# Kernel tuning notes

Measured on AMD Instinct MI355X. Metric: run time of the kernel, lower is better.

Reference implementation:

```python
import jax, jax.numpy as jnp
import numpy as np

B, L, H, E, D = 2, 2048, 8, 64, 64

def setup_inputs() -> dict:
    key = jax.random.key(0)
    kq, kk, kv, ks = jax.random.split(key, 4)
    return {
        "queries": jax.random.normal(kq, (B, L, H, E), dtype=jnp.float32),
        "keys": jax.random.normal(kk, (B, L, H, E), dtype=jnp.float32),
        "values": jax.random.normal(kv, (B, L, H, D), dtype=jnp.float32),
        "sigma": jax.random.normal(ks, (B, L, H), dtype=jnp.float32),
    }

def reference(queries, keys, values, sigma):
    b, l, h, e = queries.shape
    scale = 1.0 / np.sqrt(e).astype(np.float32)
    # raw attention scores [B,H,L,S]
    scores = jnp.einsum('blhe,bshe->bhls', queries, keys)
    # strict causal mask (mask j > i)
    causal = jnp.triu(jnp.ones((l, l), dtype=bool), k=1)
    scores = jnp.where(causal[None, None], -jnp.inf, scores)
    attn = scale * scores
    # learned Gaussian prior per query-key distance
    sig = jnp.transpose(sigma, (0, 2, 1))            # [B,H,L]
    sig = jax.nn.sigmoid(sig * 5.0) + 1e-5
    sig = jnp.power(3.0, sig) - 1.0                  # in (0, 2)
    sig = sig[..., None]                             # [B,H,L,1] broadcast over window
    idx = jnp.arange(l, dtype=jnp.float32)
    dist = jnp.abs(idx[:, None] - idx[None, :])      # [L,L]
    inv_sqrt_2pi = 1.0 / np.sqrt(2.0 * np.pi).astype(np.float32)
    prior = (inv_sqrt_2pi / sig) * jnp.exp(-(dist[None, None] ** 2) / (2.0 * sig ** 2))  # [B,H,L,L]
    series = jax.nn.softmax(attn, axis=-1)           # [B,H,L,S]
    V = jnp.einsum('bhls,bshd->blhd', series, values)  # [B,L,H,D]
    sigma_out = jnp.broadcast_to(sig, prior.shape)
    return V, series, prior, sigma_out
```

## Files before the change

kernel.cpp:

```cpp
#include <hip/hip_runtime.h>

#define B_ 2
#define L_ 2048
#define H_ 8
#define E_ 64

typedef __attribute__((ext_vector_type(8))) short short8;
typedef __attribute__((ext_vector_type(4))) float f32x4;

static constexpr size_t OFF_S = 2097152;
static constexpr size_t OFF_P = OFF_S + 67108864;
static constexpr size_t OFF_G = OFF_P + 67108864;

__device__ __forceinline__ unsigned short f2bf(float x) {
    union { float f; unsigned int u; } c; c.f = x;
    unsigned int u = c.u;
    u += 0x7fffu + ((u >> 16) & 1u);
    return (unsigned short)(u >> 16);
}

__device__ __forceinline__ void st_bf4(unsigned short* dst, float4 x) {
    union { unsigned short u[4]; uint2 v; } t;
    t.u[0] = f2bf(x.x); t.u[1] = f2bf(x.y); t.u[2] = f2bf(x.z); t.u[3] = f2bf(x.w);
    *reinterpret_cast<uint2*>(dst) = t.v;
}

__global__ __launch_bounds__(256) void attn_all(
    const float* __restrict__ q, const float* __restrict__ k,
    const float* __restrict__ v, const float* __restrict__ sg,
    float* __restrict__ out)
{
    __shared__ __attribute__((aligned(16))) unsigned short Ks[64][72];
    __shared__ __attribute__((aligned(16))) unsigned short Vt[64][72];
    __shared__ __attribute__((aligned(16))) unsigned short Pt[16][72];
    __shared__ float l_sums[16];
    __shared__ float rowA[16], rowC[16], rowSig[16];

    const int tid  = threadIdx.x;
    const int wv   = tid >> 6;
    const int lane = tid & 63;
    const int quad = lane >> 4;
    const int l16  = lane & 15;

    const int blk = blockIdx.x;
    const int s   = 127 - (blk >> 4);
    const int bh  = blk & 15;
    const int b   = bh >> 3;
    const int h   = bh & 7;
    const int i0  = s << 4;

    if (tid < 16) l_sums[tid] = 0.0f;

    short8 a0, a1;
    {
        const float* qr = q + ((size_t)((b * L_ + (i0 + l16)) * H_ + h)) * E_;
        const float4* q4 = reinterpret_cast<const float4*>(qr) + quad * 2;
        float4 x0 = q4[0], x1 = q4[1];
        float4 y0 = q4[8], y1 = q4[9];
        union { short8 v8; unsigned short u[8]; } fa, fb;
        fa.u[0]=f2bf(x0.x); fa.u[1]=f2bf(x0.y); fa.u[2]=f2bf(x0.z); fa.u[3]=f2bf(x0.w);
        fa.u[4]=f2bf(x1.x); fa.u[5]=f2bf(x1.y); fa.u[6]=f2bf(x1.z); fa.u[7]=f2bf(x1.w);
        fb.u[0]=f2bf(y0.x); fb.u[1]=f2bf(y0.y); fb.u[2]=f2bf(y0.z); fb.u[3]=f2bf(y0.w);
        fb.u[4]=f2bf(y1.x); fb.u[5]=f2bf(y1.y); fb.u[6]=f2bf(y1.z); fb.u[7]=f2bf(y1.w);
        a0 = fa.v8; a1 = fb.v8;
    }

    const int ntiles = ((i0 + 15) >> 6) + 1;
    const int jend   = ntiles << 6;

    float lpart[4] = {0.f, 0.f, 0.f, 0.f};
    for (int t = 0; t < ntiles; ++t) {
        const int j0 = t << 6;
        __syncthreads();
        {
            int r = tid >> 4;
            const int c = (tid & 15) << 2;
            #pragma unroll
            for (int p = 0; p < 4; ++p, r += 16) {
                const size_t g = ((size_t)((b * L_ + (j0 + r)) * H_ + h)) * E_ + c;
                st_bf4(&Ks[r][c], *reinterpret_cast<const float4*>(k + g));
            }
        }
        __syncthreads();
        const unsigned short* krow = &Ks[(wv << 4) + l16][0];
        short8 b0 = *reinterpret_cast<const short8*>(krow + quad * 8);
        short8 b1 = *reinterpret_cast<const short8*>(krow + 32 + quad * 8);
        f32x4 c4 = {0.f, 0.f, 0.f, 0.f};
        c4 = __builtin_amdgcn_mfma_f32_16x16x32_bf16(a0, b0, c4, 0, 0, 0);
        c4 = __builtin_amdgcn_mfma_f32_16x16x32_bf16(a1, b1, c4, 0, 0, 0);
        const int j = j0 + (wv << 4) + l16;
        #pragma unroll
        for (int r = 0; r < 4; ++r) {
            const int i = i0 + (quad << 2) + r;
            lpart[r] += (j <= i) ? __expf(c4[r] * 0.125f - 8.0f) : 0.0f;
        }
    }
    #pragma unroll
    for (int r = 0; r < 4; ++r) {
        float x = lpart[r];
        x += __shfl_xor(x, 1); x += __shfl_xor(x, 2);
        x += __shfl_xor(x, 4); x += __shfl_xor(x, 8);
        if (l16 == 0) atomicAdd(&l_sums[(quad << 2) + r], x);
    }
    __syncthreads();
    float inv[4];
    #pragma unroll
    for (int r = 0; r < 4; ++r) inv[r] = 1.0f / l_sums[(quad << 2) + r];

    f32x4 oacc = {0.f, 0.f, 0.f, 0.f};
    float* outS = out + OFF_S;
    for (int t = 0; t < ntiles; ++t) {
        const int j0 = t << 6;
        __syncthreads();
        {
            int r = tid >> 4;
            const int c = (tid & 15) << 2;
            #pragma unroll
            for (int p = 0; p < 4; ++p, r += 16) {
                const size_t g = ((size_t)((b * L_ + (j0 + r)) * H_ + h)) * E_ + c;
                st_bf4(&Ks[r][c], *reinterpret_cast<const float4*>(k + g));
                const float4 vv = *reinterpret_cast<const float4*>(v + g);
                Vt[c + 0][r] = f2bf(vv.x);
                Vt[c + 1][r] = f2bf(vv.y);
                Vt[c + 2][r] = f2bf(vv.z);
                Vt[c + 3][r] = f2bf(vv.w);
            }
        }
        __syncthreads();
        const unsigned short* krow = &Ks[(wv << 4) + l16][0];
        short8 b0 = *reinterpret_cast<const short8*>(krow + quad * 8);
        short8 b1 = *reinterpret_cast<const short8*>(krow + 32 + quad * 8);
        f32x4 c4 = {0.f, 0.f, 0.f, 0.f};
        c4 = __builtin_amdgcn_mfma_f32_16x16x32_bf16(a0, b0, c4, 0, 0, 0);
        c4 = __builtin_amdgcn_mfma_f32_16x16x32_bf16(a1, b1, c4, 0, 0, 0);
        const int j = j0 + (wv << 4) + l16;
        #pragma unroll
        for (int r = 0; r < 4; ++r) {
            const int i = i0 + (quad << 2) + r;
            float p = (j <= i) ? __expf(c4[r] * 0.125f - 8.0f) : 0.0f;
            float pn = p * inv[r];
            outS[((size_t)bh * L_ + i) * L_ + j] = pn;
            Pt[(quad << 2) + r][(wv << 4) + l16] = f2bf(pn);
        }
        __syncthreads();
        const unsigned short* prow = &Pt[l16][0];
        const unsigned short* vrow = &Vt[(wv << 4) + l16][0];
        short8 pa0 = *reinterpret_cast<const short8*>(prow + quad * 8);
        short8 pa1 = *reinterpret_cast<const short8*>(prow + 32 + quad * 8);
        short8 vb0 = *reinterpret_cast<const short8*>(vrow + quad * 8);
        short8 vb1 = *reinterpret_cast<const short8*>(vrow + 32 + quad * 8);
        oacc = __builtin_amdgcn_mfma_f32_16x16x32_bf16(pa0, vb0, oacc, 0, 0, 0);
        oacc = __builtin_amdgcn_mfma_f32_16x16x32_bf16(pa1, vb1, oacc, 0, 0, 0);
    }
    #pragma unroll
    for (int r = 0; r < 4; ++r) {
        const int i = i0 + (quad << 2) + r;
        const int d = (wv << 4) + l16;
        out[((size_t)((b * L_ + i) * H_ + h)) * 64 + d] = oacc[r];
    }

    __syncthreads();
    if (tid < 16) {
        const int i = i0 + tid;
        const float x   = sg[(size_t)(b * L_ + i) * H_ + h];
        const float sgm = 1.0f / (1.0f + __expf(-5.0f * x)) + 1e-5f;
        const float sp  = expm1f(sgm * 1.0986122886681098f);
        rowSig[tid] = sp;
        rowA[tid]   = 0.3989422804014327f / sp;
        rowC[tid]   = 0.5f / (sp * sp);
    }
    __syncthreads();
    float* outP = out + OFF_P;
    float* outG = out + OFF_G;
    for (int r = 0; r < 16; ++r) {
        const int i = i0 + r;
        const float A  = rowA[r];
        const float C2 = rowC[r];
        const float S  = rowSig[r];
        const size_t rb = ((size_t)bh * L_ + i) * L_;
        #pragma unroll
        for (int p = 0; p < 2; ++p) {
            const int c = (tid + (p << 8)) << 2;
            const float d0 = (float)(i - c);
            const float d1 = d0 - 1.0f, d2 = d0 - 2.0f, d3 = d0 - 3.0f;
            float4 pr;
            pr.x = A * __expf(-d0 * d0 * C2);
            pr.y = A * __expf(-d1 * d1 * C2);
            pr.z = A * __expf(-d2 * d2 * C2);
            pr.w = A * __expf(-d3 * d3 * C2);
            *reinterpret_cast<float4*>(outP + rb + c) = pr;
            float4 sv = {S, S, S, S};
            *reinterpret_cast<float4*>(outG + rb + c) = sv;
            if (c >= jend) {
                float4 z = {0.f, 0.f, 0.f, 0.f};
                *reinterpret_cast<float4*>(outS + rb + c) = z;
            }
        }
    }
}

extern "C" void kernel_launch(void* const* d_in, const int* in_sizes, int n_in,
                              void* d_out, int out_size, void* d_ws, size_t ws_size,
                              hipStream_t stream) {
    const float* q  = (const float*)d_in[0];
    const float* k  = (const float*)d_in[1];
    const float* v  = (const float*)d_in[2];
    const float* sg = (const float*)d_in[3];
    attn_all<<<dim3(2048), dim3(256), 0, stream>>>(q, k, v, sg, (float*)d_out);
}
```

Before: 903.8 us.

## Split into prep/attn/finish kernels with single-pass unnormalized attention and async LDS loads

Adds a prep kernel that converts K and V to swizzled bf16 tiles in workspace, so the attention kernel can double-buffer tiles with global_load_lds instead of reconverting fp32 per block. The attention kernel now makes one pass over keys, accumulating unnormalized probabilities, writing them to the series output and normalizing O at the end. A finish kernel rescales the series rows by the inverse sums and writes the prior and sigma outputs. This removes the second QK pass and the repeated K/V conversion, at the cost of re-reading and re-writing the lower-triangular series in finish and two extra launches.

```diff
diff --git a/kernel.cpp b/kernel.cpp
--- a/kernel.cpp
+++ b/kernel.cpp
@@ -1,9 +1,7 @@
 #include <hip/hip_runtime.h>
 
-#define B_ 2
 #define L_ 2048
 #define H_ 8
-#define E_ 64
 
 typedef __attribute__((ext_vector_type(8))) short short8;
 typedef __attribute__((ext_vector_type(4))) float f32x4;
@@ -11,6 +9,9 @@
 static constexpr size_t OFF_S = 2097152;
 static constexpr size_t OFF_P = OFF_S + 67108864;
 static constexpr size_t OFF_G = OFF_P + 67108864;
+
+static constexpr size_t WS_K = 1u << 20;
+static constexpr size_t WS_V = WS_K + (4u << 20);
 
 __device__ __forceinline__ unsigned short f2bf(float x) {
     union { float f; unsigned int u; } c; c.f = x;
@@ -18,23 +19,75 @@
     u += 0x7fffu + ((u >> 16) & 1u);
     return (unsigned short)(u >> 16);
 }
-
-__device__ __forceinline__ void st_bf4(unsigned short* dst, float4 x) {
-    union { unsigned short u[4]; uint2 v; } t;
-    t.u[0] = f2bf(x.x); t.u[1] = f2bf(x.y); t.u[2] = f2bf(x.z); t.u[3] = f2bf(x.w);
-    *reinterpret_cast<uint2*>(dst) = t.v;
-}
-
-__global__ __launch_bounds__(256) void attn_all(
-    const float* __restrict__ q, const float* __restrict__ k,
-    const float* __restrict__ v, const float* __restrict__ sg,
-    float* __restrict__ out)
+__device__ __forceinline__ float bf2f(unsigned short u) {
+    union { float f; unsigned int v; } c; c.v = ((unsigned int)u) << 16; return c.f;
+}
+
+__device__ __forceinline__ void gld_lds16(const unsigned short* g, unsigned short* l) {
+    __builtin_amdgcn_global_load_lds(
+        (const __attribute__((address_space(1))) void*)g,
+        (__attribute__((address_space(3))) void*)l, 16, 0, 0);
+}
+
+__global__ __launch_bounds__(256) void prep(
+    const float* __restrict__ k, const float* __restrict__ v,
+    unsigned short* __restrict__ wsK, unsigned short* __restrict__ wsV)
 {
-    __shared__ __attribute__((aligned(16))) unsigned short Ks[64][72];
-    __shared__ __attribute__((aligned(16))) unsigned short Vt[64][72];
+    const int tid = threadIdx.x;
+    const int blk = blockIdx.x;
+    __shared__ __attribute__((aligned(16))) unsigned short tr[64][72];
+    if (blk < 512) {
+        const int bh = blk >> 5, t = blk & 31;
+        const int b = bh >> 3, h = bh & 7;
+        unsigned short* dst = wsK + (size_t)(bh * 32 + t) * 4096;
+        #pragma unroll
+        for (int p = 0; p < 2; ++p) {
+            const int cid = tid + (p << 8);
+            const int r = cid >> 3, c = cid & 7;
+            const int j = (t << 6) + r;
+            const float4* src = reinterpret_cast<const float4*>(
+                k + (((size_t)((b * L_ + j) * H_ + h)) << 6) + (c << 3));
+            float4 x0 = src[0], x1 = src[1];
+            union { short8 s; unsigned short u[8]; } w;
+            w.u[0]=f2bf(x0.x); w.u[1]=f2bf(x0.y); w.u[2]=f2bf(x0.z); w.u[3]=f2bf(x0.w);
+            w.u[4]=f2bf(x1.x); w.u[5]=f2bf(x1.y); w.u[6]=f2bf(x1.z); w.u[7]=f2bf(x1.w);
+            *reinterpret_cast<short8*>(dst + r * 64 + ((c ^ (r & 7)) << 3)) = w.s;
+        }
+    } else {
+        const int vb = blk - 512;
+        const int bh = vb >> 5, t = vb & 31;
+        const int b = bh >> 3, h = bh & 7;
+        const int col4 = (tid & 15) << 2;
+        #pragma unroll
+        for (int p = 0; p < 4; ++p) {
+            const int r = (tid >> 4) + (p << 4);
+            const int j = (t << 6) + r;
+            float4 x = *reinterpret_cast<const float4*>(
+                v + (((size_t)((b * L_ + j) * H_ + h)) << 6) + col4);
+            tr[col4 + 0][r] = f2bf(x.x); tr[col4 + 1][r] = f2bf(x.y);
+            tr[col4 + 2][r] = f2bf(x.z); tr[col4 + 3][r] = f2bf(x.w);
+        }
+        __syncthreads();
+        unsigned short* dst = wsV + (size_t)(bh * 32 + t) * 4096;
+        #pragma unroll
+        for (int p = 0; p < 2; ++p) {
+            const int cid = tid + (p << 8);
+            const int d = cid >> 3, cj = cid & 7;
+            short8 s = *reinterpret_cast<const short8*>(&tr[d][cj << 3]);
+            *reinterpret_cast<short8*>(dst + d * 64 + ((cj ^ (d & 7)) << 3)) = s;
+        }
+    }
+}
+
+__global__ __launch_bounds__(256) void attn(
+    const float* __restrict__ q,
+    const unsigned short* __restrict__ wsK, const unsigned short* __restrict__ wsV,
+    float* __restrict__ out, float* __restrict__ ws_inv)
+{
+    __shared__ __attribute__((aligned(16))) unsigned short Kb[2][4096];
+    __shared__ __attribute__((aligned(16))) unsigned short Vb[2][4096];
     __shared__ __attribute__((aligned(16))) unsigned short Pt[16][72];
     __shared__ float l_sums[16];
-    __shared__ float rowA[16], rowC[16], rowSig[16];
 
     const int tid  = threadIdx.x;
     const int wv   = tid >> 6;
@@ -45,15 +98,14 @@
     const int blk = blockIdx.x;
     const int s   = 127 - (blk >> 4);
     const int bh  = blk & 15;
-    const int b   = bh >> 3;
-    const int h   = bh & 7;
+    const int b   = bh >> 3, h = bh & 7;
     const int i0  = s << 4;
 
     if (tid < 16) l_sums[tid] = 0.0f;
 
     short8 a0, a1;
     {
-        const float* qr = q + ((size_t)((b * L_ + (i0 + l16)) * H_ + h)) * E_;
+        const float* qr = q + (((size_t)((b * L_ + (i0 + l16)) * H_ + h)) << 6);
         const float4* q4 = reinterpret_cast<const float4*>(qr) + quad * 2;
         float4 x0 = q4[0], x1 = q4[1];
         float4 y0 = q4[8], y1 = q4[9];
@@ -65,136 +117,131 @@
         a0 = fa.v8; a1 = fb.v8;
     }
 
-    const int ntiles = ((i0 + 15) >> 6) + 1;
-    const int jend   = ntiles << 6;
-
+    const int ntiles = (s >> 2) + 1;
+    const unsigned short* gK = wsK + ((size_t)bh * 32) * 4096;
+    const unsigned short* gV = wsV + ((size_t)bh * 32) * 4096;
+
+    #define STAGE(buf, t) do {                                              \
+        const unsigned short* _sk = gK + (size_t)(t) * 4096;                \
+        const unsigned short* _sv = gV + (size_t)(t) * 4096;                \
+        _Pragma("unroll")                                                   \
+        for (int _qq = 0; _qq < 2; ++_qq) {                                 \
+            const int _off = (wv << 10) + (_qq << 9);                       \
+            gld_lds16(_sk + _off + (lane << 3), &Kb[buf][_off]);            \
+            gld_lds16(_sv + _off + (lane << 3), &Vb[buf][_off]);            \
+        }                                                                   \
+    } while (0)
+
+    f32x4 oacc = {0.f, 0.f, 0.f, 0.f};
     float lpart[4] = {0.f, 0.f, 0.f, 0.f};
+    float* outS = out + OFF_S;
+    const int r = (wv << 4) + l16;
+
+    STAGE(0, 0);
     for (int t = 0; t < ntiles; ++t) {
+        const int p = t & 1;
+        __syncthreads();
+        if (t + 1 < ntiles) STAGE(1 - p, t + 1);
         const int j0 = t << 6;
-        __syncthreads();
-        {
-            int r = tid >> 4;
-            const int c = (tid & 15) << 2;
-            #pragma unroll
-            for (int p = 0; p < 4; ++p, r += 16) {
-                const size_t g = ((size_t)((b * L_ + (j0 + r)) * H_ + h)) * E_ + c;
-                st_bf4(&Ks[r][c], *reinterpret_cast<const float4*>(k + g));
-            }
-        }
-        __syncthreads();
-        const unsigned short* krow = &Ks[(wv << 4) + l16][0];
-        short8 b0 = *reinterpret_cast<const short8*>(krow + quad * 8);
-        short8 b1 = *reinterpret_cast<const short8*>(krow + 32 + quad * 8);
+        short8 b0 = *reinterpret_cast<const short8*>(&Kb[p][r * 64 + ((quad ^ (r & 7)) << 3)]);
+        short8 b1 = *reinterpret_cast<const short8*>(&Kb[p][r * 64 + (((quad + 4) ^ (r & 7)) << 3)]);
         f32x4 c4 = {0.f, 0.f, 0.f, 0.f};
         c4 = __builtin_amdgcn_mfma_f32_16x16x32_bf16(a0, b0, c4, 0, 0, 0);
         c4 = __builtin_amdgcn_mfma_f32_16x16x32_bf16(a1, b1, c4, 0, 0, 0);
-        const int j = j0 + (wv << 4) + l16;
-        #pragma unroll
-        for (int r = 0; r < 4; ++r) {
-            const int i = i0 + (quad << 2) + r;
-            lpart[r] += (j <= i) ? __expf(c4[r] * 0.125f - 8.0f) : 0.0f;
-        }
-    }
+        const int j = j0 + r;
+        #pragma unroll
+        for (int rr = 0; rr < 4; ++rr) {
+            const int i = i0 + (quad << 2) + rr;
+            float pv = (j <= i) ? __expf(c4[rr] * 0.125f - 8.0f) : 0.0f;
+            lpart[rr] += pv;
+            Pt[(quad << 2) + rr][r] = f2bf(pv);
+        }
+        __syncthreads();
+        short8 pa0 = *reinterpret_cast<const short8*>(&Pt[l16][quad << 3]);
+        short8 pa1 = *reinterpret_cast<const short8*>(&Pt[l16][32 + (quad << 3)]);
+        short8 vb0 = *reinterpret_cast<const short8*>(&Vb[p][r * 64 + ((quad ^ (r & 7)) << 3)]);
+        short8 vb1 = *reinterpret_cast<const short8*>(&Vb[p][r * 64 + (((quad + 4) ^ (r & 7)) << 3)]);
+        oacc = __builtin_amdgcn_mfma_f32_16x16x32_bf16(pa0, vb0, oacc, 0, 0, 0);
+        oacc = __builtin_amdgcn_mfma_f32_16x16x32_bf16(pa1, vb1, oacc, 0, 0, 0);
+        const int srow = tid >> 4, scol = (tid & 15) << 2;
+        const unsigned short* pp = &Pt[srow][scol];
+        float4 pf = { bf2f(pp[0]), bf2f(pp[1]), bf2f(pp[2]), bf2f(pp[3]) };
+        *reinterpret_cast<float4*>(outS + (((size_t)(bh * L_ + i0 + srow)) << 11) + j0 + scol) = pf;
+    }
+    #undef STAGE
+
     #pragma unroll
-    for (int r = 0; r < 4; ++r) {
-        float x = lpart[r];
+    for (int rr = 0; rr < 4; ++rr) {
+        float x = lpart[rr];
         x += __shfl_xor(x, 1); x += __shfl_xor(x, 2);
         x += __shfl_xor(x, 4); x += __shfl_xor(x, 8);
-        if (l16 == 0) atomicAdd(&l_sums[(quad << 2) + r], x);
+        if (l16 == 0) atomicAdd(&l_sums[(quad << 2) + rr], x);
     }
     __syncthreads();
-    float inv[4];
     #pragma unroll
-    for (int r = 0; r < 4; ++r) inv[r] = 1.0f / l_sums[(quad << 2) + r];
-
-    f32x4 oacc = {0.f, 0.f, 0.f, 0.f};
+    for (int rr = 0; rr < 4; ++rr) {
+        const int i = i0 + (quad << 2) + rr;
+        const float inv = 1.0f / l_sums[(quad << 2) + rr];
+        out[(((size_t)((b * L_ + i) * H_ + h)) << 6) + (wv << 4) + l16] = oacc[rr] * inv;
+    }
+    if (tid < 16) ws_inv[(bh << 11) + i0 + tid] = 1.0f / l_sums[tid];
+}
+
+__global__ __launch_bounds__(256) void finish(
+    const float* __restrict__ sg, const float* __restrict__ ws_inv,
+    float* __restrict__ out)
+{
+    __shared__ float sA[4], sC2[4], sS[4], sI[4];
+    const int tid = threadIdx.x;
+    const int g0 = blockIdx.x << 2;
+    if (tid < 4) {
+        const int g = g0 + tid;
+        const int bh = g >> 11, i = g & 2047, b = bh >> 3, h = bh & 7;
+        const float x = sg[(size_t)((b * L_ + i) * H_ + h)];
+        const float sgm = 1.0f / (1.0f + __expf(-5.0f * x)) + 1e-5f;
+        const float sp = expm1f(sgm * 1.0986122886681098f);
+        sS[tid] = sp;
+        sA[tid] = 0.3989422804014327f / sp;
+        sC2[tid] = 0.5f / (sp * sp);
+        sI[tid] = ws_inv[g];
+    }
+    __syncthreads();
     float* outS = out + OFF_S;
-    for (int t = 0; t < ntiles; ++t) {
-        const int j0 = t << 6;
-        __syncthreads();
-        {
-            int r = tid >> 4;
-            const int c = (tid & 15) << 2;
-            #pragma unroll
-            for (int p = 0; p < 4; ++p, r += 16) {
-                const size_t g = ((size_t)((b * L_ + (j0 + r)) * H_ + h)) * E_ + c;
-                st_bf4(&Ks[r][c], *reinterpret_cast<const float4*>(k + g));
-                const float4 vv = *reinterpret_cast<const float4*>(v + g);
-                Vt[c + 0][r] = f2bf(vv.x);
-                Vt[c + 1][r] = f2bf(vv.y);
-                Vt[c + 2][r] = f2bf(vv.z);
-                Vt[c + 3][r] = f2bf(vv.w);
-            }
-        }
-        __syncthreads();
-        const unsigned short* krow = &Ks[(wv << 4) + l16][0];
-        short8 b0 = *reinterpret_cast<const short8*>(krow + quad * 8);
-        short8 b1 = *reinterpret_cast<const short8*>(krow + 32 + quad * 8);
-        f32x4 c4 = {0.f, 0.f, 0.f, 0.f};
-        c4 = __builtin_amdgcn_mfma_f32_16x16x32_bf16(a0, b0, c4, 0, 0, 0);
-        c4 = __builtin_amdgcn_mfma_f32_16x16x32_bf16(a1, b1, c4, 0, 0, 0);
-        const int j = j0 + (wv << 4) + l16;
-        #pragma unroll
-        for (int r = 0; r < 4; ++r) {
-            const int i = i0 + (quad << 2) + r;
-            float p = (j <= i) ? __expf(c4[r] * 0.125f - 8.0f) : 0.0f;
-            float pn = p * inv[r];
-            outS[((size_t)bh * L_ + i) * L_ + j] = pn;
-            Pt[(quad << 2) + r][(wv << 4) + l16] = f2bf(pn);
-        }
-        __syncthreads();
-        const unsigned short* prow = &Pt[l16][0];
-        const unsigned short* vrow = &Vt[(wv << 4) + l16][0];
-        short8 pa0 = *reinterpret_cast<const short8*>(prow + quad * 8);
-        short8 pa1 = *reinterpret_cast<const short8*>(prow + 32 + quad * 8);
-        short8 vb0 = *reinterpret_cast<const short8*>(vrow + quad * 8);
-        short8 vb1 = *reinterpret_cast<const short8*>(vrow + 32 + quad * 8);
-        oacc = __builtin_amdgcn_mfma_f32_16x16x32_bf16(pa0, vb0, oacc, 0, 0, 0);
-        oacc = __builtin_amdgcn_mfma_f32_16x16x32_bf16(pa1, vb1, oacc, 0, 0, 0);
-    }
-    #pragma unroll
-    for (int r = 0; r < 4; ++r) {
-        const int i = i0 + (quad << 2) + r;
-        const int d = (wv << 4) + l16;
-        out[((size_t)((b * L_ + i) * H_ + h)) * 64 + d] = oacc[r];
-    }
-
-    __syncthreads();
-    if (tid < 16) {
-        const int i = i0 + tid;
-        const float x   = sg[(size_t)(b * L_ + i) * H_ + h];
-        const float sgm = 1.0f / (1.0f + __expf(-5.0f * x)) + 1e-5f;
-        const float sp  = expm1f(sgm * 1.0986122886681098f);
-        rowSig[tid] = sp;
-        rowA[tid]   = 0.3989422804014327f / sp;
-        rowC[tid]   = 0.5f / (sp * sp);
-    }
-    __syncthreads();
     float* outP = out + OFF_P;
     float* outG = out + OFF_G;
-    for (int r = 0; r < 16; ++r) {
-        const int i = i0 + r;
-        const float A  = rowA[r];
-        const float C2 = rowC[r];
-        const float S  = rowSig[r];
-        const size_t rb = ((size_t)bh * L_ + i) * L_;
+    #pragma unroll
+    for (int rr = 0; rr < 4; ++rr) {
+        const int g = g0 + rr;
+        const int i = g & 2047;
+        const size_t base = (size_t)g << 11;
+        const float A = sA[rr], C2 = sC2[rr], S = sS[rr], I = sI[rr];
         #pragma unroll
         for (int p = 0; p < 2; ++p) {
             const int c = (tid + (p << 8)) << 2;
             const float d0 = (float)(i - c);
-            const float d1 = d0 - 1.0f, d2 = d0 - 2.0f, d3 = d0 - 3.0f;
+            const float d1 = d0 - 1.f, d2 = d0 - 2.f, d3 = d0 - 3.f;
             float4 pr;
             pr.x = A * __expf(-d0 * d0 * C2);
             pr.y = A * __expf(-d1 * d1 * C2);
             pr.z = A * __expf(-d2 * d2 * C2);
             pr.w = A * __expf(-d3 * d3 * C2);
-            *reinterpret_cast<float4*>(outP + rb + c) = pr;
+            *reinterpret_cast<float4*>(outP + base + c) = pr;
             float4 sv = {S, S, S, S};
-            *reinterpret_cast<float4*>(outG + rb + c) = sv;
-            if (c >= jend) {
-                float4 z = {0.f, 0.f, 0.f, 0.f};
-                *reinterpret_cast<float4*>(outS + rb + c) = z;
+            *reinterpret_cast<float4*>(outG + base + c) = sv;
+            float4 se;
+            if (c + 3 <= i) {
+                se = *reinterpret_cast<const float4*>(outS + base + c);
+                se.x *= I; se.y *= I; se.z *= I; se.w *= I;
+            } else if (c > i) {
+                se.x = 0.f; se.y = 0.f; se.z = 0.f; se.w = 0.f;
+            } else {
+                const float4 t4 = *reinterpret_cast<const float4*>(outS + base + c);
+                se.x = (c     <= i) ? t4.x * I : 0.f;
+                se.y = (c + 1 <= i) ? t4.y * I : 0.f;
+                se.z = (c + 2 <= i) ? t4.z * I : 0.f;
+                se.w = (c + 3 <= i) ? t4.w * I : 0.f;
             }
+            *reinterpret_cast<float4*>(outS + base + c) = se;
         }
     }
 }
@@ -206,5 +253,11 @@
     const float* k  = (const float*)d_in[1];
     const float* v  = (const float*)d_in[2];
     const float* sg = (const float*)d_in[3];
-    attn_all<<<dim3(2048), dim3(256), 0, stream>>>(q, k, v, sg, (float*)d_out);
-}
+    float* outp = (float*)d_out;
+    float* ws_inv = (float*)d_ws;
+    unsigned short* wsK = (unsigned short*)((char*)d_ws + WS_K);
+    unsigned short* wsV = (unsigned short*)((char*)d_ws + WS_V);
+    prep<<<dim3(1024), dim3(256), 0, stream>>>(k, v, wsK, wsV);
+    attn<<<dim3(2048), dim3(256), 0, stream>>>(q, wsK, wsV, outp, ws_inv);
+    finish<<<dim3(8192), dim3(256), 0, stream>>>(sg, ws_inv, outp);
+}
```

Result: no change. 892.2 us (-1.3%).
